# Performance work log

Measured on AMD Instinct MI355X. Metric: run time of the kernel, lower is better.

Reference implementation:

```python
import jax, jax.numpy as jnp
import numpy as np

B, S, E, H, T = 32, 512, 768, 128, 15  # H = hidden per direction (hidden_dim//2)


def setup_inputs() -> dict:
    key = jax.random.key(0)
    ks = jax.random.split(key, 16)
    sc = 1.0 / np.sqrt(H)
    inp = {
        "x": jax.random.normal(ks[0], (B, S, E), dtype=jnp.float32),
        "tags": jax.random.randint(ks[1], (B, S), 0, T),
        "mask": jnp.ones((B, S), dtype=jnp.int32),
        # forward-direction LSTM params (PyTorch gate order i,f,g,o)
        "Wih_f": jax.random.uniform(ks[2], (4 * H, E), minval=-sc, maxval=sc),
        "Whh_f": jax.random.uniform(ks[3], (4 * H, H), minval=-sc, maxval=sc),
        "bih_f": jax.random.uniform(ks[4], (4 * H,), minval=-sc, maxval=sc),
        "bhh_f": jax.random.uniform(ks[5], (4 * H,), minval=-sc, maxval=sc),
        # backward-direction LSTM params
        "Wih_b": jax.random.uniform(ks[6], (4 * H, E), minval=-sc, maxval=sc),
        "Whh_b": jax.random.uniform(ks[7], (4 * H, H), minval=-sc, maxval=sc),
        "bih_b": jax.random.uniform(ks[8], (4 * H,), minval=-sc, maxval=sc),
        "bhh_b": jax.random.uniform(ks[9], (4 * H,), minval=-sc, maxval=sc),
        # projection 2H -> T
        "Wp": jax.random.uniform(ks[10], (T, 2 * H), minval=-sc, maxval=sc),
        "bp": jax.random.uniform(ks[11], (T,), minval=-sc, maxval=sc),
        # CRF params (torchcrf: uniform(-0.1, 0.1))
        "trans": jax.random.uniform(ks[12], (T, T), minval=-0.1, maxval=0.1),
        "start_t": jax.random.uniform(ks[13], (T,), minval=-0.1, maxval=0.1),
        "end_t": jax.random.uniform(ks[14], (T,), minval=-0.1, maxval=0.1),
    }
    return inp


def _lstm_dir(xs, Wih, Whh, bih, bhh):
    """Single-direction LSTM over xs: (S, B, E) -> (S, B, H)."""
    h0 = jnp.zeros((xs.shape[1], Whh.shape[1]), xs.dtype)

    def step(carry, xt):
        h, c = carry
        z = xt @ Wih.T + h @ Whh.T + (bih + bhh)  # (B, 4H)
        i, f, g, o = jnp.split(z, 4, axis=-1)
        c = jax.nn.sigmoid(f) * c + jax.nn.sigmoid(i) * jnp.tanh(g)
        h = jax.nn.sigmoid(o) * jnp.tanh(c)
        return (h, c), h

    _, hs = jax.lax.scan(step, (h0, h0), xs)
    return hs


def _crf_nll(em, tg, mk, trans, start_t, end_t):
    """Negative log-likelihood, sum-reduced. em:(S,B,T) tg:(S,B) mk:(S,B) float."""
    b_idx = jnp.arange(em.shape[1])
    # --- numerator: score of the gold path ---
    em_tag = jnp.take_along_axis(em, tg[..., None], axis=2)[..., 0]  # (S, B)
    score = start_t[tg[0]] + em_tag[0]
    trans_sc = trans[tg[:-1], tg[1:]]  # (S-1, B)
    score = score + ((trans_sc + em_tag[1:]) * mk[1:]).sum(axis=0)
    seq_ends = mk.astype(jnp.int32).sum(axis=0) - 1  # (B,)
    last_tags = tg[seq_ends, b_idx]
    score = score + end_t[last_tags]
    # --- denominator: log partition via forward algorithm (scan) ---
    def fstep(alpha, inp):
        em_t, m_t = inp  # (B,T), (B,)
        nxt = jax.nn.logsumexp(alpha[:, :, None] + trans[None] + em_t[:, None, :], axis=1)
        alpha = jnp.where(m_t[:, None] > 0, nxt, alpha)
        return alpha, None

    alpha0 = start_t[None, :] + em[0]  # (B, T)
    alpha, _ = jax.lax.scan(fstep, alpha0, (em[1:], mk[1:]))
    logZ = jax.nn.logsumexp(alpha + end_t[None, :], axis=1)  # (B,)
    return -(score - logZ).sum()


def reference(x, tags, mask, Wih_f, Whh_f, bih_f, bhh_f, Wih_b, Whh_b, bih_b, bhh_b, Wp, bp, trans, start_t, end_t):
    xs = jnp.transpose(x, (1, 0, 2))  # (S, B, E)
    hf = _lstm_dir(xs, Wih_f, Whh_f, bih_f, bhh_f)
    hb = _lstm_dir(xs[::-1], Wih_b, Whh_b, bih_b, bhh_b)[::-1]
    h = jnp.concatenate([hf, hb], axis=-1)  # (S, B, 2H)
    em = h @ Wp.T + bp  # emissions (S, B, T)
    tg = tags.T  # (S, B)
    mk = mask.T.astype(em.dtype)
    return _crf_nll(em, tg, mk, trans, start_t, end_t)
```

## Files before the change

kernel.cpp:

```cpp
#include <hip/hip_runtime.h>
#include <hip/hip_bf16.h>
#include <cstdint>

typedef __attribute__((ext_vector_type(8))) short short8;
typedef __attribute__((ext_vector_type(4))) float f32x4;

#define NS 512
#define NB 32
#define NE 768
#define NH 128
#define NT 15
#define NM (NB*NS)

#define LOG2E  1.4426950408889634f
#define LOG2E2 2.8853900817779268f

__device__ __forceinline__ float bflo(unsigned int u){ return __builtin_bit_cast(float, u << 16); }
__device__ __forceinline__ float bfhi(unsigned int u){ return __builtin_bit_cast(float, u & 0xffff0000u); }
__device__ __forceinline__ float bfu(unsigned short u){ return __builtin_bit_cast(float, (unsigned)u << 16); }

__device__ __forceinline__ float rcpf_(float x){
#if __has_builtin(__builtin_amdgcn_rcpf)
  return __builtin_amdgcn_rcpf(x);
#else
  return __fdividef(1.f, x);
#endif
}
__device__ __forceinline__ float ex2_(float x){
#if __has_builtin(__builtin_amdgcn_exp2f)
  return __builtin_amdgcn_exp2f(x);
#else
  return exp2f(x);
#endif
}

__device__ __forceinline__ void lds_barrier() {
  asm volatile("s_waitcnt lgkmcnt(0)" ::: "memory");
  __builtin_amdgcn_s_barrier();
  asm volatile("" ::: "memory");
}

__device__ __forceinline__ void gload16(const void* g, void* l) {
#if __has_builtin(__builtin_amdgcn_global_load_lds)
  __builtin_amdgcn_global_load_lds((const __attribute__((address_space(1))) void*)g,
                                   (__attribute__((address_space(3))) void*)l, 16, 0, 0);
#else
  *(uint4*)l = *(const uint4*)g;
#endif
}

__global__ void cvt_bf16_kernel(const float* __restrict__ in,
                                __hip_bfloat16* __restrict__ out, int n4) {
  int i = blockIdx.x*blockDim.x + threadIdx.x;
  int stride = gridDim.x*blockDim.x;
  for (int j = i; j < n4; j += stride) {
    float4 v = ((const float4*)in)[j];
    ushort4 o;
    o.x = __builtin_bit_cast(unsigned short, __float2bfloat16(v.x));
    o.y = __builtin_bit_cast(unsigned short, __float2bfloat16(v.y));
    o.z = __builtin_bit_cast(unsigned short, __float2bfloat16(v.z));
    o.w = __builtin_bit_cast(unsigned short, __float2bfloat16(v.w));
    ((ushort4*)out)[j] = o;
  }
}

__global__ void prep_weights_kernel(
    const float* __restrict__ wihf, const float* __restrict__ wihb,
    const float* __restrict__ whhf, const float* __restrict__ whhb,
    const float* __restrict__ bihf, const float* __restrict__ bhhf,
    const float* __restrict__ bihb, const float* __restrict__ bhhb,
    __hip_bfloat16* __restrict__ wihp,
    __hip_bfloat16* __restrict__ whhp,
    float* __restrict__ biasp)
{
  const int n = blockIdx.x;
  const int dir = n >> 9, cc = n & 511, j = cc >> 2, g = cc & 3;
  const float fac = (g == 2) ? LOG2E2 : LOG2E;
  const int srow = g*128 + j;
  const float* si = (dir ? wihb : wihf) + (size_t)srow*768;
  __hip_bfloat16* di = wihp + (size_t)n*768;
  for (int e = threadIdx.x; e < 768; e += 256) di[e] = __float2bfloat16(si[e]*fac);
  const float* sh = (dir ? whhb : whhf) + (size_t)srow*128;
  __hip_bfloat16* dh = whhp + (size_t)n*128;
  if (threadIdx.x < 128) dh[threadIdx.x] = __float2bfloat16(sh[threadIdx.x]*fac);
  if (threadIdx.x == 0)
    biasp[n] = fac * (dir ? (bihb[srow] + bhhb[srow]) : (bihf[srow] + bhhf[srow]));
}

__global__ __launch_bounds__(256, 4) void gemm_xproj(
    const __hip_bfloat16* __restrict__ A,
    const __hip_bfloat16* __restrict__ Bw,
    const float* __restrict__ biasp,
    __hip_bfloat16* __restrict__ xqd)
{
  __shared__ __align__(16) __hip_bfloat16 As[128*64];
  __shared__ __align__(16) __hip_bfloat16 Bs[128*64];
  const int bm = blockIdx.x * 128;
  const int bn = blockIdx.y * 128;
  const int tid = threadIdx.x;
  const int lane = tid & 63;
  const int wv = tid >> 6;
  const int wr = wv >> 1, wc = wv & 1;
  char* AsB = (char*)As;
  char* BsB = (char*)Bs;
  const char* Ab = (const char*)A;
  const char* Bb = (const char*)Bw;
  f32x4 acc[4][4] = {};

  for (int kt = 0; kt < 12; ++kt) {
    const int k0 = kt * 64;
    __syncthreads();
    #pragma unroll
    for (int i = 0; i < 4; ++i) {
      int fb = i*4096 + tid*16;
      int r  = fb >> 7;
      int cb = fb & 127;
      gload16(Ab + ((size_t)(bm + r)*768 + k0)*2 + cb, AsB + fb);
      gload16(Bb + ((size_t)(bn + r)*768 + k0)*2 + cb, BsB + fb);
    }
    __syncthreads();
    #pragma unroll
    for (int ks = 0; ks < 2; ++ks) {
      const int krow = ks*32 + ((lane >> 4) << 3);
      short8 af[4], bfr[4];
      #pragma unroll
      for (int m = 0; m < 4; ++m) {
        int row = wr*64 + m*16 + (lane & 15);
        af[m] = *(const short8*)(AsB + (row*64 + krow)*2);
      }
      #pragma unroll
      for (int n = 0; n < 4; ++n) {
        int row = wc*64 + n*16 + (lane & 15);
        bfr[n] = *(const short8*)(BsB + (row*64 + krow)*2);
      }
      #pragma unroll
      for (int m = 0; m < 4; ++m)
        #pragma unroll
        for (int n = 0; n < 4; ++n)
          acc[m][n] = __builtin_amdgcn_mfma_f32_16x16x32_bf16(af[m], bfr[n], acc[m][n], 0, 0, 0);
    }
  }
  #pragma unroll
  for (int m = 0; m < 4; ++m) {
    #pragma unroll
    for (int n = 0; n < 4; ++n) {
      const int col = bn + wc*64 + n*16 + (lane & 15);
      const float bv = biasp[col];
      const int dir = col >> 9;
      const int cc  = col & 511;
      #pragma unroll
      for (int jj = 0; jj < 4; ++jj) {
        const int row = bm + wr*64 + m*16 + ((lane >> 4)*4 + jj);
        xqd[((size_t)dir*NM + row)*512 + cc] = __float2bfloat16(acc[m][n][jj] + bv);
      }
    }
  }
}

__global__ __launch_bounds__(512) __attribute__((amdgpu_waves_per_eu(1, 2)))
void lstm_mfma(
    const __hip_bfloat16* __restrict__ xqd,
    const __hip_bfloat16* __restrict__ whhp,
    unsigned short* __restrict__ hf,
    unsigned short* __restrict__ hb)
{
  __shared__ __align__(16) char hfrag[2*4224];
  __shared__ __align__(16) float z_lds[4*520];

  const int bid = blockIdx.x;
  const int dir = bid >> 3, bg = bid & 7;
  const int t = threadIdx.x;
  const int w = t >> 6, l = t & 63;
  const int ln = l & 15, lp = l >> 4;

  uint4 afu[4][4];
  {
    const char* wbase = (const char*)(whhp + (size_t)dir*512*128);
    #pragma unroll
    for (int r = 0; r < 4; ++r) {
      const int row = (w*4 + r)*16 + ln;
      #pragma unroll
      for (int kc = 0; kc < 4; ++kc)
        afu[r][kc] = *(const uint4*)(wbase + ((size_t)row*128 + lp*8 + kc*32)*2);
    }
  }

  for (int i = t; i < 2*4224/4; i += 512) ((int*)hfrag)[i] = 0;

  const int b4 = t & 3, j = t >> 2;
  const int bsafe = bg*4 + b4;
  const int jsw = j ^ ((j >> 3) & 7);
  const int woff = (j >> 5)*1056 + ((j >> 3) & 3)*256 + b4*16 + (j & 7)*2;
  const int sdir = dir ? -1 : 1;
  const int s0 = dir ? 511 : 0;
  const ptrdiff_t xstep = (ptrdiff_t)sdir*512;
  const ptrdiff_t hstep = (ptrdiff_t)sdir*128;
  const __hip_bfloat16* xbase = xqd + ((size_t)dir*NM + (size_t)bsafe*512)*512
                                + (ptrdiff_t)s0*512 + j*4;
  unsigned short* hout = (dir ? hb : hf) + (size_t)bsafe*512*128 + (ptrdiff_t)s0*128 + j;

  float c = 0.f;

  uint2 x0 = *(const uint2*)(xbase);
  uint2 x1 = *(const uint2*)(xbase + xstep);
  uint2 x2 = *(const uint2*)(xbase + 2*xstep);
  uint2 x3 = *(const uint2*)(xbase + 3*xstep);
  const __hip_bfloat16* xpre = xbase + 4*xstep;
  __syncthreads();

  int buf = 0;

  auto STEP = [&](uint2& xc, bool pf) {
    short8 bfv[4];
    #pragma unroll
    for (int kc = 0; kc < 4; ++kc)
      bfv[kc] = *(const short8*)(hfrag + buf*4224 + kc*1056 + l*16);

    f32x4 acc[4];
    #pragma unroll
    for (int r = 0; r < 4; ++r) {
      acc[r] = f32x4{0.f, 0.f, 0.f, 0.f};
      #pragma unroll
      for (int kc = 0; kc < 4; ++kc)
        acc[r] = __builtin_amdgcn_mfma_f32_16x16x32_bf16(
                   __builtin_bit_cast(short8, afu[r][kc]), bfv[kc], acc[r], 0, 0, 0);
    }

    if (ln < 4) {
      #pragma unroll
      for (int r = 0; r < 4; ++r) {
        const int jw = (w*4 + r)*4 + lp;
        const int js = jw ^ ((jw >> 3) & 7);
        *(f32x4*)&z_lds[ln*520 + 4*js] = acc[r];
      }
    }
    lds_barrier();

    const f32x4 zv = *(const f32x4*)&z_lds[b4*520 + 4*jsw];
    const float zi = zv[0] + bflo(xc.x);
    const float zf = zv[1] + bfhi(xc.x);
    const float zg = zv[2] + bflo(xc.y);
    const float zo = zv[3] + bfhi(xc.y);
    const float I = rcpf_(1.f + ex2_(-zi));
    const float F = rcpf_(1.f + ex2_(-zf));
    const float G = 1.f - 2.f*rcpf_(ex2_(zg) + 1.f);
    const float O = rcpf_(1.f + ex2_(-zo));
    c = F*c + I*G;
    const float h = O*(1.f - 2.f*rcpf_(ex2_(c*LOG2E2) + 1.f));

    const unsigned short hbits =
        __builtin_bit_cast(unsigned short, __float2bfloat16(h));
    *(short*)(hfrag + (buf ^ 1)*4224 + woff) = (short)hbits;
    *hout = hbits;
    hout += hstep;

    if (pf) { xc = *(const uint2*)xpre; xpre += xstep; }
    lds_barrier();
    buf ^= 1;
  };

  for (int it = 0; it < 127; ++it) {
    #pragma unroll
    for (int r = 0; r < 4; ++r)
      #pragma unroll
      for (int kc = 0; kc < 4; ++kc)
        asm volatile("" : "+a"(afu[r][kc].x), "+a"(afu[r][kc].y),
                          "+a"(afu[r][kc].z), "+a"(afu[r][kc].w));
    STEP(x0, true);
    STEP(x1, true);
    STEP(x2, true);
    STEP(x3, true);
  }
  STEP(x0, false);
  STEP(x1, false);
  STEP(x2, false);
  STEP(x3, false);
}

__global__ __launch_bounds__(128) void em_kernel(
    const unsigned short* __restrict__ hf, const unsigned short* __restrict__ hb,
    const float* __restrict__ Wp, const float* __restrict__ bp,
    float* __restrict__ em)
{
  __shared__ float wps[15*256];
  __shared__ float bps[15];
  const int tid = threadIdx.x;
  for (int i = tid; i < 15*256; i += 128) wps[i] = Wp[i];
  if (tid < 15) bps[tid] = bp[tid];
  __syncthreads();
  const size_t m = (size_t)blockIdx.x*128 + tid;
  float acc[15];
  #pragma unroll
  for (int t2 = 0; t2 < 15; ++t2) acc[t2] = bps[t2];
  const ushort4* hf4 = (const ushort4*)(hf + m*128);
  const ushort4* hb4 = (const ushort4*)(hb + m*128);
  for (int kc = 0; kc < 32; ++kc) {
    const ushort4 hv = hf4[kc];
    const float h0 = bfu(hv.x), h1 = bfu(hv.y), h2 = bfu(hv.z), h3 = bfu(hv.w);
    #pragma unroll
    for (int t2 = 0; t2 < 15; ++t2)
      acc[t2] += h0*wps[t2*256 + kc*4+0] + h1*wps[t2*256 + kc*4+1]
               + h2*wps[t2*256 + kc*4+2] + h3*wps[t2*256 + kc*4+3];
  }
  for (int kc = 0; kc < 32; ++kc) {
    const ushort4 hv = hb4[kc];
    const float h0 = bfu(hv.x), h1 = bfu(hv.y), h2 = bfu(hv.z), h3 = bfu(hv.w);
    #pragma unroll
    for (int t2 = 0; t2 < 15; ++t2)
      acc[t2] += h0*wps[t2*256 + 128 + kc*4+0] + h1*wps[t2*256 + 128 + kc*4+1]
               + h2*wps[t2*256 + 128 + kc*4+2] + h3*wps[t2*256 + 128 + kc*4+3];
  }
  float* eo = em + m*15;
  #pragma unroll
  for (int t2 = 0; t2 < 15; ++t2) eo[t2] = acc[t2];
}

__global__ __launch_bounds__(64) void crf_kernel(
    const float* __restrict__ em,
    const int* __restrict__ tags, const int* __restrict__ mask,
    const float* __restrict__ trans, const float* __restrict__ start_t,
    const float* __restrict__ end_t, float* __restrict__ nllb)
{
  __shared__ __align__(16) float ems[512*15];
  __shared__ float trs[225];
  __shared__ int tgs[512];
  __shared__ int mks[512];
  const int b = blockIdx.x, j = threadIdx.x;
  const float* emb = em + (size_t)b*512*15;
  {
    const float4* s4 = (const float4*)emb;
    float4* d4 = (float4*)ems;
    for (int i = j; i < 512*15/4; i += 64) d4[i] = s4[i];
    for (int i = j; i < 512; i += 64) { tgs[i] = tags[b*512+i]; mks[i] = mask[b*512+i]; }
    for (int i = j; i < 225; i += 64) trs[i] = trans[i];
  }
  __syncthreads();

  float trc[15];
  #pragma unroll
  for (int i = 0; i < 15; ++i) trc[i] = (j < 15) ? trs[i*15 + j] : 0.f;

  float alpha = (j < 15) ? (start_t[j] + ems[j]) : -3.0e38f;
  for (int s = 1; s < 512; ++s) {
    const float emv = (j < 15) ? ems[s*15 + j] : 0.f;
    const int msk = mks[s];
    float v[15];
    #pragma unroll
    for (int i = 0; i < 15; ++i) {
#if __has_builtin(__builtin_amdgcn_readlane)
      const float ai = __builtin_bit_cast(float,
          __builtin_amdgcn_readlane(__builtin_bit_cast(int, alpha), i));
#else
      const float ai = __shfl(alpha, i, 64);
#endif
      v[i] = ai + trc[i];
    }
    const float t01 = fmaxf(v[0], v[1]),  t23 = fmaxf(v[2], v[3]);
    const float t45 = fmaxf(v[4], v[5]),  t67 = fmaxf(v[6], v[7]);
    const float t89 = fmaxf(v[8], v[9]),  tab = fmaxf(v[10], v[11]);
    const float tcd = fmaxf(v[12], v[13]);
    const float q0 = fmaxf(t01, t23), q1 = fmaxf(t45, t67);
    const float q2 = fmaxf(t89, tab), q3 = fmaxf(tcd, v[14]);
    const float mx = fmaxf(fmaxf(q0, q1), fmaxf(q2, q3));
    float e[15];
    #pragma unroll
    for (int i = 0; i < 15; ++i) e[i] = __expf(v[i] - mx);
    const float s01 = e[0]+e[1], s23 = e[2]+e[3], s45 = e[4]+e[5], s67 = e[6]+e[7];
    const float s89 = e[8]+e[9], sab = e[10]+e[11], scd = e[12]+e[13];
    const float u0 = s01+s23, u1 = s45+s67, u2 = s89+sab, u3 = scd+e[14];
    const float sum = (u0+u1) + (u2+u3);
    const float nxt = emv + mx + __logf(sum);
    if (msk > 0 && j < 15) alpha = nxt;
  }
  float vz = (j < 15) ? (alpha + end_t[j]) : -3.0e38f;
  float mz = vz;
  #pragma unroll
  for (int off = 32; off > 0; off >>= 1) mz = fmaxf(mz, __shfl_xor(mz, off, 64));
  float se = (j < 15) ? __expf(vz - mz) : 0.f;
  #pragma unroll
  for (int off = 32; off > 0; off >>= 1) se += __shfl_xor(se, off, 64);
  const float logZ = mz + __logf(se);

  float sc = 0.f; int cnt = 0;
  for (int s = j; s < 512; s += 64) cnt += (mks[s] ? 1 : 0);
  for (int s = 1 + j; s < 512; s += 64) {
    if (mks[s]) {
      const int tp = tgs[s-1], tc = tgs[s];
      sc += trs[tp*15 + tc] + ems[s*15 + tc];
    }
  }
  #pragma unroll
  for (int off = 32; off > 0; off >>= 1) {
    sc  += __shfl_xor(sc, off, 64);
    cnt += __shfl_xor(cnt, off, 64);
  }
  if (j == 0) {
    const int t0 = tgs[0];
    sc += start_t[t0] + ems[t0];
    int last = cnt - 1; if (last < 0) last = 0;
    sc += end_t[tgs[last]];
    nllb[b] = logZ - sc;
  }
}

__global__ __launch_bounds__(64) void nll_reduce_kernel(const float* __restrict__ nllb,
                                                        float* __restrict__ out) {
  const int j = threadIdx.x;
  float v = (j < 32) ? nllb[j] : 0.f;
  #pragma unroll
  for (int off = 32; off > 0; off >>= 1) v += __shfl_xor(v, off, 64);
  if (j == 0) out[0] = v;
}

extern "C" void kernel_launch(void* const* d_in, const int* in_sizes, int n_in,
                              void* d_out, int out_size, void* d_ws, size_t ws_size,
                              hipStream_t stream) {
  const float* x      = (const float*)d_in[0];
  const int*   tags   = (const int*)d_in[1];
  const int*   mask   = (const int*)d_in[2];
  const float* Wih_f  = (const float*)d_in[3];
  const float* Whh_f  = (const float*)d_in[4];
  const float* bih_f  = (const float*)d_in[5];
  const float* bhh_f  = (const float*)d_in[6];
  const float* Wih_b  = (const float*)d_in[7];
  const float* Whh_b  = (const float*)d_in[8];
  const float* bih_b  = (const float*)d_in[9];
  const float* bhh_b  = (const float*)d_in[10];
  const float* Wp     = (const float*)d_in[11];
  const float* bp     = (const float*)d_in[12];
  const float* trans  = (const float*)d_in[13];
  const float* start_t= (const float*)d_in[14];
  const float* end_t  = (const float*)d_in[15];
  float* out = (float*)d_out;

  char* ws = (char*)d_ws;
  size_t off = 0;
  auto alloc = [&](size_t bytes) { char* p = ws + off; off += (bytes + 255) & ~(size_t)255; return p; };
  __hip_bfloat16* xbf   = (__hip_bfloat16*)alloc((size_t)NM*NE*2);
  __hip_bfloat16* Wihbf = (__hip_bfloat16*)alloc((size_t)1024*NE*2);
  __hip_bfloat16* whhp  = (__hip_bfloat16*)alloc((size_t)2*512*128*2);
  float*          biasp = (float*)alloc(1024*4);
  __hip_bfloat16* xqd   = (__hip_bfloat16*)alloc((size_t)2*NM*512*2);
  unsigned short* hf    = (unsigned short*)alloc((size_t)NM*128*2);
  unsigned short* hb    = (unsigned short*)alloc((size_t)NM*128*2);
  float*          em    = (float*)alloc((size_t)NM*15*4);
  float*          nllb  = (float*)alloc(32*4);
  (void)ws_size; (void)in_sizes; (void)n_in; (void)out_size;

  cvt_bf16_kernel<<<2048, 256, 0, stream>>>(x, xbf, NM*NE/4);
  prep_weights_kernel<<<1024, 256, 0, stream>>>(Wih_f, Wih_b, Whh_f, Whh_b,
                                                bih_f, bhh_f, bih_b, bhh_b,
                                                Wihbf, whhp, biasp);

  gemm_xproj<<<dim3(128, 8), 256, 0, stream>>>(xbf, Wihbf, biasp, xqd);
  lstm_mfma<<<16, 512, 0, stream>>>(xqd, whhp, hf, hb);
  em_kernel<<<128, 128, 0, stream>>>(hf, hb, Wp, bp, em);
  crf_kernel<<<32, 64, 0, stream>>>(em, tags, mask, trans, start_t, end_t, nllb);
  nll_reduce_kernel<<<1, 64, 0, stream>>>(nllb, out);
}
```

Before: 590.2 us.

## Parallelize CRF forward recursion via chunked log-semiring matrix products

The serial 511-step CRF forward scan is split into 32 chunks of 16 steps. Each chunk computes a 15x15 log-semiring transfer matrix in parallel across 1024 blocks, and a final kernel chains the 32 matrices per sequence. This is meant to shorten the long serial latency chain, at the cost of about 15x more arithmetic, an extra launch and a pmat buffer. The GEMM grid is also flattened with a block-index swizzle to improve L2 locality.

```diff
diff --git a/kernel.cpp b/kernel.cpp
--- a/kernel.cpp
+++ b/kernel.cpp
@@ -46,6 +46,14 @@
                                    (__attribute__((address_space(3))) void*)l, 16, 0, 0);
 #else
   *(uint4*)l = *(const uint4*)g;
+#endif
+}
+
+__device__ __forceinline__ float rdlane(float v, int i){
+#if __has_builtin(__builtin_amdgcn_readlane)
+  return __builtin_bit_cast(float, __builtin_amdgcn_readlane(__builtin_bit_cast(int, v), i));
+#else
+  return __shfl(v, i, 64);
 #endif
 }
 
@@ -95,8 +103,10 @@
 {
   __shared__ __align__(16) __hip_bfloat16 As[128*64];
   __shared__ __align__(16) __hip_bfloat16 Bs[128*64];
-  const int bm = blockIdx.x * 128;
-  const int bn = blockIdx.y * 128;
+  const int id  = blockIdx.x;
+  const int swz = (id & 7)*128 + (id >> 3);
+  const int bm = (swz >> 3) * 128;
+  const int bn = (swz & 7) * 128;
   const int tid = threadIdx.x;
   const int lane = tid & 63;
   const int wv = tid >> 6;
@@ -315,14 +325,74 @@
   for (int t2 = 0; t2 < 15; ++t2) eo[t2] = acc[t2];
 }
 
-__global__ __launch_bounds__(64) void crf_kernel(
+__global__ __launch_bounds__(64) void crf_chunks(
     const float* __restrict__ em,
+    const int* __restrict__ mask,
+    const float* __restrict__ trans,
+    float* __restrict__ pmat)
+{
+  __shared__ float trs[240];
+  __shared__ float cur[2][15][16];
+  __shared__ float emc[16][16];
+  __shared__ int mkc[16];
+  const int b = blockIdx.x, cix = blockIdx.y;
+  const int t = threadIdx.x;
+  const int s0 = 1 + cix*16;
+  const int ns = (512 - s0 < 16) ? (512 - s0) : 16;
+
+  for (int e = t; e < 225; e += 64) trs[(e/15)*16 + (e%15)] = trans[e];
+  for (int e = t; e < ns*15; e += 64) {
+    const int k = e/15, j = e%15;
+    emc[k][j] = em[((size_t)b*512 + s0 + k)*15 + j];
+  }
+  if (t < ns) mkc[t] = mask[b*512 + s0 + t];
+  for (int e = t; e < 225; e += 64) {
+    const int i = e/15, j = e%15;
+    cur[0][i][j] = (i == j) ? 0.f : -1e30f;
+  }
+  __syncthreads();
+
+  int cb = 0;
+  for (int k = 0; k < ns; ++k) {
+    if (mkc[k]) {
+      for (int e = t; e < 225; e += 64) {
+        const int i = e/15, j = e%15;
+        float v[15];
+        #pragma unroll
+        for (int k2 = 0; k2 < 15; ++k2) v[k2] = cur[cb][i][k2] + trs[k2*16 + j];
+        const float a01 = fmaxf(v[0], v[1]),  a23 = fmaxf(v[2], v[3]);
+        const float a45 = fmaxf(v[4], v[5]),  a67 = fmaxf(v[6], v[7]);
+        const float a89 = fmaxf(v[8], v[9]),  aab = fmaxf(v[10], v[11]);
+        const float acd = fmaxf(v[12], v[13]);
+        const float q0 = fmaxf(a01, a23), q1 = fmaxf(a45, a67);
+        const float q2 = fmaxf(a89, aab), q3 = fmaxf(acd, v[14]);
+        const float mx = fmaxf(fmaxf(q0, q1), fmaxf(q2, q3));
+        float sum = 0.f;
+        #pragma unroll
+        for (int k2 = 0; k2 < 15; ++k2) sum += __expf(v[k2] - mx);
+        cur[cb ^ 1][i][j] = emc[k][j] + mx + __logf(sum);
+      }
+      __syncthreads();
+      cb ^= 1;
+    }
+  }
+  float* P = pmat + ((size_t)b*32 + cix)*240;
+  for (int e = t; e < 225; e += 64) {
+    const int i = e/15, j = e%15;
+    P[i*16 + j] = cur[cb][i][j];
+  }
+}
+
+__global__ __launch_bounds__(64) void crf_final(
+    const float* __restrict__ em,
+    const float* __restrict__ pmat,
     const int* __restrict__ tags, const int* __restrict__ mask,
     const float* __restrict__ trans, const float* __restrict__ start_t,
     const float* __restrict__ end_t, float* __restrict__ nllb)
 {
   __shared__ __align__(16) float ems[512*15];
   __shared__ float trs[225];
+  __shared__ float Pl[240];
   __shared__ int tgs[512];
   __shared__ int mks[512];
   const int b = blockIdx.x, j = threadIdx.x;
@@ -336,43 +406,34 @@
   }
   __syncthreads();
 
-  float trc[15];
-  #pragma unroll
-  for (int i = 0; i < 15; ++i) trc[i] = (j < 15) ? trs[i*15 + j] : 0.f;
-
-  float alpha = (j < 15) ? (start_t[j] + ems[j]) : -3.0e38f;
-  for (int s = 1; s < 512; ++s) {
-    const float emv = (j < 15) ? ems[s*15 + j] : 0.f;
-    const int msk = mks[s];
+  const int jc = (j < 15) ? j : 0;
+  float alpha = (j < 15) ? (start_t[j] + ems[j]) : -1e30f;
+  for (int cix = 0; cix < 32; ++cix) {
+    const float* P = pmat + ((size_t)b*32 + cix)*240;
+    __syncthreads();
+    for (int e = j; e < 240; e += 64) Pl[e] = P[e];
+    __syncthreads();
     float v[15];
     #pragma unroll
     for (int i = 0; i < 15; ++i) {
-#if __has_builtin(__builtin_amdgcn_readlane)
-      const float ai = __builtin_bit_cast(float,
-          __builtin_amdgcn_readlane(__builtin_bit_cast(int, alpha), i));
-#else
-      const float ai = __shfl(alpha, i, 64);
-#endif
-      v[i] = ai + trc[i];
-    }
-    const float t01 = fmaxf(v[0], v[1]),  t23 = fmaxf(v[2], v[3]);
-    const float t45 = fmaxf(v[4], v[5]),  t67 = fmaxf(v[6], v[7]);
-    const float t89 = fmaxf(v[8], v[9]),  tab = fmaxf(v[10], v[11]);
-    const float tcd = fmaxf(v[12], v[13]);
-    const float q0 = fmaxf(t01, t23), q1 = fmaxf(t45, t67);
-    const float q2 = fmaxf(t89, tab), q3 = fmaxf(tcd, v[14]);
+      const float ai = rdlane(alpha, i);
+      v[i] = ai + Pl[i*16 + jc];
+    }
+    const float a01 = fmaxf(v[0], v[1]),  a23 = fmaxf(v[2], v[3]);
+    const float a45 = fmaxf(v[4], v[5]),  a67 = fmaxf(v[6], v[7]);
+    const float a89 = fmaxf(v[8], v[9]),  aab = fmaxf(v[10], v[11]);
+    const float acd = fmaxf(v[12], v[13]);
+    const float q0 = fmaxf(a01, a23), q1 = fmaxf(a45, a67);
+    const float q2 = fmaxf(a89, aab), q3 = fmaxf(acd, v[14]);
     const float mx = fmaxf(fmaxf(q0, q1), fmaxf(q2, q3));
-    float e[15];
-    #pragma unroll
-    for (int i = 0; i < 15; ++i) e[i] = __expf(v[i] - mx);
-    const float s01 = e[0]+e[1], s23 = e[2]+e[3], s45 = e[4]+e[5], s67 = e[6]+e[7];
-    const float s89 = e[8]+e[9], sab = e[10]+e[11], scd = e[12]+e[13];
-    const float u0 = s01+s23, u1 = s45+s67, u2 = s89+sab, u3 = scd+e[14];
-    const float sum = (u0+u1) + (u2+u3);
-    const float nxt = emv + mx + __logf(sum);
-    if (msk > 0 && j < 15) alpha = nxt;
-  }
-  float vz = (j < 15) ? (alpha + end_t[j]) : -3.0e38f;
+    float sum = 0.f;
+    #pragma unroll
+    for (int i = 0; i < 15; ++i) sum += __expf(v[i] - mx);
+    const float nxt = mx + __logf(sum);
+    if (j < 15) alpha = nxt;
+  }
+
+  float vz = (j < 15) ? (alpha + end_t[j]) : -1e30f;
   float mz = vz;
   #pragma unroll
   for (int off = 32; off > 0; off >>= 1) mz = fmaxf(mz, __shfl_xor(mz, off, 64));
@@ -444,6 +505,7 @@
   unsigned short* hf    = (unsigned short*)alloc((size_t)NM*128*2);
   unsigned short* hb    = (unsigned short*)alloc((size_t)NM*128*2);
   float*          em    = (float*)alloc((size_t)NM*15*4);
+  float*          pmat  = (float*)alloc((size_t)32*32*240*4);
   float*          nllb  = (float*)alloc(32*4);
   (void)ws_size; (void)in_sizes; (void)n_in; (void)out_size;
 
@@ -452,9 +514,10 @@
                                                 bih_f, bhh_f, bih_b, bhh_b,
                                                 Wihbf, whhp, biasp);
 
-  gemm_xproj<<<dim3(128, 8), 256, 0, stream>>>(xbf, Wihbf, biasp, xqd);
+  gemm_xproj<<<1024, 256, 0, stream>>>(xbf, Wihbf, biasp, xqd);
   lstm_mfma<<<16, 512, 0, stream>>>(xqd, whhp, hf, hb);
   em_kernel<<<128, 128, 0, stream>>>(hf, hb, Wp, bp, em);
-  crf_kernel<<<32, 64, 0, stream>>>(em, tags, mask, trans, start_t, end_t, nllb);
+  crf_chunks<<<dim3(32, 32), 64, 0, stream>>>(em, mask, trans, pmat);
+  crf_final<<<32, 64, 0, stream>>>(em, pmat, tags, mask, trans, start_t, end_t, nllb);
   nll_reduce_kernel<<<1, 64, 0, stream>>>(nllb, out);
 }
```

After: 503.5 us. 14.7% less time.
